# Kernel tuning notes

Measured on AMD Instinct MI355X. Metric: run time of the kernel, lower is better.

The kernel has to match this reference:

```python
import jax, jax.numpy as jnp
import numpy as np

BLOCK = 8

def _dct_matrix(N: int) -> jnp.ndarray:
    # DCT-II orthonormal matrix, matches the torch double loop
    k = np.arange(N)[:, None]
    n = np.arange(N)[None, :]
    mat = np.sqrt(2.0 / N) * np.cos(np.pi * k * (2 * n + 1) / (2 * N))
    mat[0, :] = np.sqrt(1.0 / N)
    return jnp.asarray(mat, dtype=jnp.float32)

def _haar_dwt(x):
    x00 = x[:, :, 0::2, 0::2]
    x01 = x[:, :, 0::2, 1::2]
    x10 = x[:, :, 1::2, 0::2]
    x11 = x[:, :, 1::2, 1::2]
    LL = (x00 + x01 + x10 + x11) * 0.5
    LH = (x00 + x01 - x10 - x11) * 0.5
    HL = (x00 - x01 + x10 - x11) * 0.5
    HH = (x00 - x01 - x10 + x11) * 0.5
    return LL, LH, HL, HH

def _block_dct2(x, D):
    # x: [B,C,H,W] -> blockwise 2D DCT with BLOCK x BLOCK tiles
    B, C, H, W = x.shape
    bs = BLOCK
    blocks = x.reshape(B, C, H // bs, bs, W // bs, bs)
    blocks = blocks.transpose(0, 1, 2, 4, 3, 5)  # [B,C,Hb,Wb,bs,bs]
    out = jnp.einsum('km,bchwmn,ln->bchwkl', D, blocks, D)  # D @ X @ D^T
    out = out.transpose(0, 1, 2, 4, 3, 5).reshape(B, C, H, W)
    return out

def setup_inputs() -> dict:
    key = jax.random.key(0)
    x = jax.random.normal(key, (16, 3, 1024, 1024), dtype=jnp.float32)
    return {"x": x}

def reference(x):
    D = _dct_matrix(BLOCK)
    LL, LH, HL, HH = _haar_dwt(x)
    LL_dct = _block_dct2(LL, D)
    return (LL_dct, LH, HL, HH)
```

## Files before the change

### kernel.cpp

```cpp
#include <hip/hip_runtime.h>
#include <math.h>


#define H_IN   1024
#define W_IN   1024
#define H_HALF 512
#define W_HALF 512
#define NIMG   48
#define NOUT   ((size_t)NIMG * H_HALF * W_HALF)

__global__ __launch_bounds__(256) void hfe_kernel(const float* __restrict__ x,
                                                  float* __restrict__ out) {
    __shared__ float Dm[8][8];
    __shared__ float M[8][65];
    __shared__ float T[8][65];

    const int t = threadIdx.x;

    if (t < 64) {
        const int k = t >> 3, n = t & 7;
        double v = (k == 0) ? 0.35355339059327376220
                            : 0.5 * cos(M_PI * (double)(k * (2 * n + 1)) / 16.0);
        Dm[k][n] = (float)v;
    }

    const int bid = blockIdx.x;
    const int bc  = bid >> 9;
    const int rem = bid & 511;
    const int ty  = rem >> 3;
    const int tx  = rem & 7;

    const int hr = t >> 5;
    const int cp = t & 31;

    const int in_row = ty * 16 + hr * 2;
    const int in_col = tx * 128 + cp * 4;
    const float* base = x + (size_t)bc * (H_IN * W_IN);

    const float4 a = *(const float4*)(base + (size_t)in_row * W_IN + in_col);
    const float4 b = *(const float4*)(base + (size_t)(in_row + 1) * W_IN + in_col);

    const float ll0 = (a.x + a.y + b.x + b.y) * 0.5f;
    const float lh0 = (a.x + a.y - b.x - b.y) * 0.5f;
    const float hl0 = (a.x - a.y + b.x - b.y) * 0.5f;
    const float hh0 = (a.x - a.y - b.x + b.y) * 0.5f;
    const float ll1 = (a.z + a.w + b.z + b.w) * 0.5f;
    const float lh1 = (a.z + a.w - b.z - b.w) * 0.5f;
    const float hl1 = (a.z - a.w + b.z - b.w) * 0.5f;
    const float hh1 = (a.z - a.w - b.z + b.w) * 0.5f;

    const int h_row = ty * 8 + hr;
    const int h_col = tx * 64 + cp * 2;
    const size_t hidx = (size_t)bc * ((size_t)H_HALF * W_HALF)
                      + (size_t)h_row * W_HALF + h_col;

    *(float2*)(out + NOUT     + hidx) = make_float2(lh0, lh1);
    *(float2*)(out + 2 * NOUT + hidx) = make_float2(hl0, hl1);
    *(float2*)(out + 3 * NOUT + hidx) = make_float2(hh0, hh1);

    M[hr][cp * 2]     = ll0;
    M[hr][cp * 2 + 1] = ll1;

    __syncthreads();

    {
        const int blk = cp >> 2;
        const int l0  = (cp * 2) & 7;
        const float* mrow = &M[hr][blk * 8];
        float t0 = 0.f, t1 = 0.f;
#pragma unroll
        for (int n = 0; n < 8; ++n) {
            const float mv = mrow[n];
            t0 += mv * Dm[l0][n];
            t1 += mv * Dm[l0 + 1][n];
        }
        T[hr][cp * 2]     = t0;
        T[hr][cp * 2 + 1] = t1;
    }

    __syncthreads();

    {
        float o0 = 0.f, o1 = 0.f;
#pragma unroll
        for (int m = 0; m < 8; ++m) {
            const float dk = Dm[hr][m];
            o0 += dk * T[m][cp * 2];
            o1 += dk * T[m][cp * 2 + 1];
        }
        *(float2*)(out + hidx) = make_float2(o0, o1);
    }
}

extern "C" void kernel_launch(void* const* d_in, const int* in_sizes, int n_in,
                              void* d_out, int out_size, void* d_ws, size_t ws_size,
                              hipStream_t stream) {
    const float* x = (const float*)d_in[0];
    float* out = (float*)d_out;
    hfe_kernel<<<dim3(NIMG * 64 * 8), dim3(256), 0, stream>>>(x, out);
}
```

Before: 323.7 us.

## Process full 8-wide DCT block per thread with compile-time row transform

Each thread now loads 16 input columns across two rows and computes eight Haar outputs per band. It does the row DCT in registers using a constexpr coefficient table, so the first shared-memory stage and one barrier go away. The column DCT reads float4 tiles from shared memory, and all outputs are written as float4. Each block covers a 16x128 output tile, cutting the grid to a quarter of its former size. This should raise per-thread work and memory-access width, at the cost of more registers and fewer blocks in flight.

```diff
diff --git a/kernel.cpp b/kernel.cpp
--- a/kernel.cpp
+++ b/kernel.cpp
@@ -2,18 +2,35 @@
 #include <math.h>
 
 
-#define H_IN   1024
-#define W_IN   1024
-#define H_HALF 512
-#define W_HALF 512
-#define NIMG   48
-#define NOUT   ((size_t)NIMG * H_HALF * W_HALF)
+#define NOUT ((size_t)48 * 512 * 512)
+
+#define C0 0.35355339059327376f
+#define C1 0.49039264020161522f
+#define C2 0.46193976625564337f
+#define C3 0.41573480615127262f
+#define C4 0.35355339059327376f
+#define C5 0.27778511650980111f
+#define C6 0.19134171618254489f
+#define C7 0.09754516100806414f
+
+#define LD4(dst, src) do { float4 _v = *(const float4*)(src); \
+    (dst)[0]=_v.x; (dst)[1]=_v.y; (dst)[2]=_v.z; (dst)[3]=_v.w; } while(0)
 
 __global__ __launch_bounds__(256) void hfe_kernel(const float* __restrict__ x,
                                                   float* __restrict__ out) {
-    __shared__ float Dm[8][8];
-    __shared__ float M[8][65];
-    __shared__ float T[8][65];
+    static constexpr float DMc[8][8] = {
+        { C0,  C0,  C0,  C0,  C0,  C0,  C0,  C0},
+        { C1,  C3,  C5,  C7, -C7, -C5, -C3, -C1},
+        { C2,  C6, -C6, -C2, -C2, -C6,  C6,  C2},
+        { C3, -C7, -C1, -C5,  C5,  C1,  C7, -C3},
+        { C4, -C4, -C4,  C4,  C4, -C4, -C4,  C4},
+        { C5, -C1,  C7,  C3, -C3, -C7,  C1, -C5},
+        { C6, -C2,  C2, -C6, -C6,  C2, -C2,  C6},
+        { C7, -C5,  C3, -C1,  C1, -C3,  C5, -C7},
+    };
+
+    __shared__ float4 T4[16][33];
+    __shared__ float  Dm[8][8];
 
     const int t = threadIdx.x;
 
@@ -25,71 +42,85 @@
     }
 
     const int bid = blockIdx.x;
-    const int bc  = bid >> 9;
-    const int rem = bid & 511;
-    const int ty  = rem >> 3;
-    const int tx  = rem & 7;
+    const int bc  = bid >> 7;
+    const int rem = bid & 127;
+    const int ty  = rem >> 2;
+    const int tx  = rem & 3;
 
-    const int hr = t >> 5;
-    const int cp = t & 31;
+    const size_t img_in  = (size_t)bc * (1024 * 1024);
+    const size_t img_out = (size_t)bc * (512 * 512);
 
-    const int in_row = ty * 16 + hr * 2;
-    const int in_col = tx * 128 + cp * 4;
-    const float* base = x + (size_t)bc * (H_IN * W_IN);
+    const int hr   = t >> 4;
+    const int bcol = t & 15;
 
-    const float4 a = *(const float4*)(base + (size_t)in_row * W_IN + in_col);
-    const float4 b = *(const float4*)(base + (size_t)(in_row + 1) * W_IN + in_col);
+    const int in_row = ty * 32 + hr * 2;
+    const int in_col = tx * 256 + bcol * 16;
+    const float* p0 = x + img_in + (size_t)in_row * 1024 + in_col;
+    const float* p1 = p0 + 1024;
 
-    const float ll0 = (a.x + a.y + b.x + b.y) * 0.5f;
-    const float lh0 = (a.x + a.y - b.x - b.y) * 0.5f;
-    const float hl0 = (a.x - a.y + b.x - b.y) * 0.5f;
-    const float hh0 = (a.x - a.y - b.x + b.y) * 0.5f;
-    const float ll1 = (a.z + a.w + b.z + b.w) * 0.5f;
-    const float lh1 = (a.z + a.w - b.z - b.w) * 0.5f;
-    const float hl1 = (a.z - a.w + b.z - b.w) * 0.5f;
-    const float hh1 = (a.z - a.w - b.z + b.w) * 0.5f;
+    float e[16], o[16];
+    LD4(&e[0], p0 + 0); LD4(&e[4], p0 + 4); LD4(&e[8], p0 + 8); LD4(&e[12], p0 + 12);
+    LD4(&o[0], p1 + 0); LD4(&o[4], p1 + 4); LD4(&o[8], p1 + 8); LD4(&o[12], p1 + 12);
 
-    const int h_row = ty * 8 + hr;
-    const int h_col = tx * 64 + cp * 2;
-    const size_t hidx = (size_t)bc * ((size_t)H_HALF * W_HALF)
-                      + (size_t)h_row * W_HALF + h_col;
+    float ll[8], lh[8], hl[8], hh[8];
+#pragma unroll
+    for (int n = 0; n < 8; ++n) {
+        const float s1 = e[2*n] + e[2*n+1], d1 = e[2*n] - e[2*n+1];
+        const float s2 = o[2*n] + o[2*n+1], d2 = o[2*n] - o[2*n+1];
+        ll[n] = (s1 + s2) * 0.5f;
+        lh[n] = (s1 - s2) * 0.5f;
+        hl[n] = (d1 + d2) * 0.5f;
+        hh[n] = (d1 - d2) * 0.5f;
+    }
 
-    *(float2*)(out + NOUT     + hidx) = make_float2(lh0, lh1);
-    *(float2*)(out + 2 * NOUT + hidx) = make_float2(hl0, hl1);
-    *(float2*)(out + 3 * NOUT + hidx) = make_float2(hh0, hh1);
+    const int h_row = ty * 16 + hr;
+    const int h_col = tx * 128 + bcol * 8;
+    float* ob = out + img_out + (size_t)h_row * 512 + h_col;
+    *(float4*)(ob + NOUT)         = make_float4(lh[0], lh[1], lh[2], lh[3]);
+    *(float4*)(ob + NOUT + 4)     = make_float4(lh[4], lh[5], lh[6], lh[7]);
+    *(float4*)(ob + 2 * NOUT)     = make_float4(hl[0], hl[1], hl[2], hl[3]);
+    *(float4*)(ob + 2 * NOUT + 4) = make_float4(hl[4], hl[5], hl[6], hl[7]);
+    *(float4*)(ob + 3 * NOUT)     = make_float4(hh[0], hh[1], hh[2], hh[3]);
+    *(float4*)(ob + 3 * NOUT + 4) = make_float4(hh[4], hh[5], hh[6], hh[7]);
 
-    M[hr][cp * 2]     = ll0;
-    M[hr][cp * 2 + 1] = ll1;
+    float tr[8];
+#pragma unroll
+    for (int l = 0; l < 8; ++l) {
+        float acc = ll[0] * DMc[l][0];
+#pragma unroll
+        for (int n = 1; n < 8; ++n) acc = fmaf(ll[n], DMc[l][n], acc);
+        tr[l] = acc;
+    }
+    T4[hr][bcol * 2]     = make_float4(tr[0], tr[1], tr[2], tr[3]);
+    T4[hr][bcol * 2 + 1] = make_float4(tr[4], tr[5], tr[6], tr[7]);
 
     __syncthreads();
 
-    {
-        const int blk = cp >> 2;
-        const int l0  = (cp * 2) & 7;
-        const float* mrow = &M[hr][blk * 8];
-        float t0 = 0.f, t1 = 0.f;
+    const int orow = t >> 4;
+    const int bc2  = t & 15;
+    const int brow = orow >> 3;
+    const int k    = orow & 7;
+
+    float Dk[8];
 #pragma unroll
-        for (int n = 0; n < 8; ++n) {
-            const float mv = mrow[n];
-            t0 += mv * Dm[l0][n];
-            t1 += mv * Dm[l0 + 1][n];
-        }
-        T[hr][cp * 2]     = t0;
-        T[hr][cp * 2 + 1] = t1;
+    for (int m = 0; m < 8; ++m) Dk[m] = Dm[k][m];
+
+    float4 a0 = make_float4(0.f, 0.f, 0.f, 0.f);
+    float4 a1 = a0;
+#pragma unroll
+    for (int m = 0; m < 8; ++m) {
+        const float dk = Dk[m];
+        const float4 t0 = T4[brow * 8 + m][bc2 * 2];
+        const float4 t1 = T4[brow * 8 + m][bc2 * 2 + 1];
+        a0.x = fmaf(dk, t0.x, a0.x); a0.y = fmaf(dk, t0.y, a0.y);
+        a0.z = fmaf(dk, t0.z, a0.z); a0.w = fmaf(dk, t0.w, a0.w);
+        a1.x = fmaf(dk, t1.x, a1.x); a1.y = fmaf(dk, t1.y, a1.y);
+        a1.z = fmaf(dk, t1.z, a1.z); a1.w = fmaf(dk, t1.w, a1.w);
     }
 
-    __syncthreads();
-
-    {
-        float o0 = 0.f, o1 = 0.f;
-#pragma unroll
-        for (int m = 0; m < 8; ++m) {
-            const float dk = Dm[hr][m];
-            o0 += dk * T[m][cp * 2];
-            o1 += dk * T[m][cp * 2 + 1];
-        }
-        *(float2*)(out + hidx) = make_float2(o0, o1);
-    }
+    float* oc = out + img_out + (size_t)(ty * 16 + orow) * 512 + tx * 128 + bc2 * 8;
+    *(float4*)(oc)     = a0;
+    *(float4*)(oc + 4) = a1;
 }
 
 extern "C" void kernel_launch(void* const* d_in, const int* in_sizes, int n_in,
@@ -97,5 +128,5 @@
                               hipStream_t stream) {
     const float* x = (const float*)d_in[0];
     float* out = (float*)d_out;
-    hfe_kernel<<<dim3(NIMG * 64 * 8), dim3(256), 0, stream>>>(x, out);
+    hfe_kernel<<<dim3(6144), dim3(256), 0, stream>>>(x, out);
 }
```

Result: slower. 331.3 us (+2.4%).
